# Kernel optimization log

Hardware: AMD Instinct MI355X
Metric: run time of the kernel (lower is better)

## Reference

```python
import jax, jax.numpy as jnp
import numpy as np

B, C, H, W = 64, 2048, 18, 9
INF = 1e9  # larger than any |cost| here (costs are -cosine sims in [-1,1])


def hungarian(cost):
    """Exact O(n^3) Jonker-Volgenant assignment (minimize total cost).
    cost: [n, n] float. Returns int32 [n]: column assigned to each row.
    Matches scipy.optimize.linear_sum_assignment on a square matrix.
    Uses 1-based indexing with a virtual row/column 0 (e-maxx formulation)."""
    n = cost.shape[0]
    costp = jnp.zeros((n + 1, n + 1), cost.dtype).at[1:, 1:].set(cost)
    jr = jnp.arange(n + 1)

    def assign_row(i, carry):
        u, v, p = carry          # u,v: dual potentials; p[j] = row matched to col j
        p = p.at[0].set(i)
        way0 = jnp.zeros(n + 1, jnp.int32)
        minv0 = jnp.full(n + 1, INF, cost.dtype)
        used0 = jnp.zeros(n + 1, bool)

        def cond(st):
            return ~st[6]

        def body(st):
            u, v, way, minv, used, j0, done = st
            used = used.at[j0].set(True)
            i0 = p[j0]
            cur = costp[i0] - u[i0] - v                  # reduced costs of row i0, vectorized over cols
            valid = (~used) & (jr >= 1)
            better = valid & (cur < minv)
            minv = jnp.where(better, cur, minv)
            way = jnp.where(better, j0, way)
            mv = jnp.where(valid, minv, INF)
            j1 = jnp.argmin(mv).astype(jnp.int32)
            delta = mv[j1]
            add = jnp.where(used, delta, jnp.zeros((), cost.dtype))
            u = u.at[p].add(add)                          # used cols have distinct p; unused add 0
            v = v - add
            minv = jnp.where(used, minv, minv - delta)
            return u, v, way, minv, used, j1, p[j1] == 0

        u, v, way, _, _, j0, _ = jax.lax.while_loop(
            cond, body, (u, v, way0, minv0, used0, jnp.int32(0), jnp.array(False)))

        def body2(st):
            j0, p = st
            j1 = way[j0]
            return j1, p.at[j0].set(p[j1])

        _, p = jax.lax.while_loop(lambda st: st[0] != 0, body2, (j0, p))
        return u, v, p

    u = jnp.zeros(n + 1, cost.dtype)
    v = jnp.zeros(n + 1, cost.dtype)
    p = jnp.zeros(n + 1, jnp.int32)
    u, v, p = jax.lax.fori_loop(1, n + 1, assign_row, (u, v, p))
    rowcol = jnp.zeros(n + 1, jnp.int32).at[p[1:]].set(jnp.arange(1, n + 1, dtype=jnp.int32))
    return rowcol[1:] - 1


def compute_mask(feat):
    b, c, h, w = feat.shape
    norms = jnp.linalg.norm(feat, axis=1).reshape(b, h * w)
    norms = norms - norms.min(axis=-1, keepdims=True)
    norms = norms / (norms.max(axis=-1, keepdims=True) + 1e-12)
    return jax.lax.stop_gradient(norms.reshape(b, 1, h, w))


def feature_similarity(fq, fk):
    b, c, h, w = fq.shape
    fq = fq.reshape(b, c, h * w)
    fk = fk.reshape(b, c, h * w)
    # F.normalize(dim=1): x / max(||x||, eps)
    nq = fq / jnp.maximum(jnp.linalg.norm(fq, axis=1, keepdims=True), 1e-12)
    nk = fk / jnp.maximum(jnp.linalg.norm(fk, axis=1, keepdims=True), 1e-12)
    return jnp.einsum('bcn,bcm->bnm', nq, nk)  # [b, n, n]


def setup_inputs() -> dict:
    key = jax.random.key(0)
    k1, k2, k3 = jax.random.split(key, 3)
    feat2d = jax.random.normal(k1, (B, C, H, W), dtype=jnp.float32)
    pos_ind = jax.random.randint(k2, (B,), 0, B, dtype=jnp.int64 if jax.config.jax_enable_x64 else jnp.int32).astype(jnp.int32)
    neg_ind = jax.random.randint(k3, (B,), 0, B, dtype=jnp.int32)
    return {"feat2d": feat2d, "pos_ind": pos_ind, "neg_ind": neg_ind}


def reference(feat2d, pos_ind, neg_ind):
    b, c, h, w = feat2d.shape
    n = h * w
    p = n // 2
    mask = compute_mask(feat2d)                         # [b,1,h,w], detached
    maskTr = mask.reshape(b, 1, n)
    s = jnp.sort(maskTr, axis=2)
    thr = s[:, :, p:p + 1]
    bMask = jnp.where(maskTr < thr, 0.0, 1.0).reshape(mask.shape)  # keep top half
    featMasked = feat2d * jax.lax.stop_gradient(bMask)
    featPos = feat2d[pos_ind]
    simPos = feature_similarity(featMasked, featPos)    # [b, n, n]
    # scipy linear_sum_assignment(sim, maximize=True) == minimize(-sim); indices are constants
    cols = jax.vmap(hungarian)(jax.lax.stop_gradient(-simPos))     # [b, n]
    assigned = jnp.take_along_axis(simPos, cols[:, :, None], axis=2)[..., 0]  # [b, n]
    pos_dis = 1.0 - assigned.sum(axis=-1) / p
    return jnp.mean(pos_dis)
```

## Files before the change

kernel.cpp:

```cpp
#include <hip/hip_runtime.h>
#include <hip/hip_bf16.h>

#define Bn 64
#define Cn 2048
#define Nn 162
#define Pn 81
#define NP 176
#define INFV 1.0e9f
#define BIGI 0x7FFFFFFF
#define RBW 328
#define ARRCAP 700

#define OFF_T    0
#define OFF_P    11534336
#define OFF_QS   (OFF_P + 64*32*192)
#define OFF_KS   (OFF_QS + 64*162)
#define OFF_COST (OFF_KS + 64*162)
#define OFF_PD   (OFF_COST + 64*162*162)

typedef __attribute__((ext_vector_type(8))) short bf16x8;
typedef __attribute__((ext_vector_type(4))) float f32x4;
typedef __attribute__((ext_vector_type(4))) unsigned u32x4;

static __device__ __forceinline__ unsigned short f2bf(float x) {
    unsigned int u = __builtin_bit_cast(unsigned int, x);
    unsigned int r = (u + 0x7fffu + ((u >> 16) & 1u)) >> 16;
    return (unsigned short)r;
}
static __device__ __forceinline__ unsigned short f2h(float x) {
    _Float16 h = (_Float16)x;
    return __builtin_bit_cast(unsigned short, h);
}
static __device__ __forceinline__ float h2f(unsigned short u) {
    return (float)__builtin_bit_cast(_Float16, u);
}
static __device__ __forceinline__ unsigned umin32(unsigned a, unsigned b) { return a < b ? a : b; }
static __device__ __forceinline__ unsigned umax32(unsigned a, unsigned b) { return a > b ? a : b; }
static __device__ __forceinline__ unsigned packnn(float v, int id) {
    float c = fmaxf(v, 0.f);
    return (__builtin_bit_cast(unsigned, c) & 0xFFFFFF00u) | (unsigned)id;
}
static __device__ __forceinline__ float unpacknn(unsigned pk) {
    return __builtin_bit_cast(float, pk & 0xFFFFFF00u);
}
static __device__ __forceinline__ unsigned reduceMin64(unsigned x) {
    int v = (int)x, t;
    t = __builtin_amdgcn_update_dpp(0, v, 0x121, 0xF, 0xF, true); v = (int)umin32((unsigned)v, (unsigned)t);
    t = __builtin_amdgcn_update_dpp(0, v, 0x122, 0xF, 0xF, true); v = (int)umin32((unsigned)v, (unsigned)t);
    t = __builtin_amdgcn_update_dpp(0, v, 0x124, 0xF, 0xF, true); v = (int)umin32((unsigned)v, (unsigned)t);
    t = __builtin_amdgcn_update_dpp(0, v, 0x128, 0xF, 0xF, true); v = (int)umin32((unsigned)v, (unsigned)t);
    unsigned a = (unsigned)__builtin_amdgcn_readlane(v, 0);
    unsigned b = (unsigned)__builtin_amdgcn_readlane(v, 16);
    unsigned c = (unsigned)__builtin_amdgcn_readlane(v, 32);
    unsigned d = (unsigned)__builtin_amdgcn_readlane(v, 48);
    return umin32(umin32(a, b), umin32(c, d));
}
static __device__ __forceinline__ int rlanei(int v, int l) { return __builtin_amdgcn_readlane(v, l); }
static __device__ __forceinline__ float rlanef(float v, int l) {
    return __builtin_bit_cast(float, __builtin_amdgcn_readlane(__builtin_bit_cast(int, v), l));
}
static __device__ __forceinline__ int laneOf(int id) { return id < 128 ? (id >> 1) : (id - 128); }
static __device__ __forceinline__ int slotOf(int id) { return id < 128 ? (id & 1) : 2; }
static __device__ __forceinline__ unsigned long long mask_n(int n) {
    if (n <= 0) return 0ull;
    if (n >= 64) return ~0ull;
    return (1ull << n) - 1ull;
}
#define SEL3(s, a0, a1, a2) ((s) == 0 ? (a0) : ((s) == 1 ? (a1) : (a2)))

__global__ __launch_bounds__(256) void k_tr(const float* __restrict__ feat, float* __restrict__ ws) {
    int x = blockIdx.x;
    int cc = x / 3, ct = x % 3;
    int b = blockIdx.y;
    int tid = threadIdx.x;
    int col = tid & 63, pg = tid >> 6;
    __shared__ unsigned Tp[32][65];
    __shared__ float Pp[4][64];
    int gc = ct * 64 + col;
    bool okc = (gc < Nn);
    const float* fbase = feat + ((size_t)b * Cn + (size_t)cc * 64) * Nn + gc;
    float s = 0.f;
    #pragma unroll
    for (int it = 0; it < 8; ++it) {
        int p = pg + it * 4;
        float v0 = okc ? fbase[(size_t)(2 * p) * Nn] : 0.f;
        float v1 = okc ? fbase[(size_t)(2 * p + 1) * Nn] : 0.f;
        s = fmaf(v0, v0, fmaf(v1, v1, s));
        Tp[p][col] = (unsigned)f2bf(v0) | ((unsigned)f2bf(v1) << 16);
    }
    Pp[pg][col] = s;
    __syncthreads();
    if (tid < 64) {
        float t0 = Pp[0][tid] + Pp[1][tid];
        float t1 = Pp[2][tid] + Pp[3][tid];
        ws[OFF_P + ((size_t)b * 32 + cc) * 192 + ct * 64 + tid] = t0 + t1;
    }
    unsigned* ft = (unsigned*)(ws + OFF_T);
    #pragma unroll
    for (int it = 0; it < 8; ++it) {
        int idx = it * 256 + tid;
        int c2 = idx >> 5, p = idx & 31;
        int gcol = ct * 64 + c2;
        if (gcol < NP) {
            ft[(size_t)(b * NP + gcol) * 1024 + cc * 32 + p] = Tp[p][c2];
        }
    }
}

__global__ void k_stats(float* __restrict__ ws) {
    int b = blockIdx.x;
    int t = threadIdx.x;
    __shared__ float arr[Nn];
    __shared__ float thr;
    float norm = 0.f;
    if (t < Nn) {
        float s = 0.f;
        #pragma unroll
        for (int ch = 0; ch < 32; ++ch) s += ws[OFF_P + ((size_t)b * 32 + ch) * 192 + t];
        norm = sqrtf(s);
        arr[t] = norm;
    }
    __syncthreads();
    float mn = INFV, mx = -INFV;
    for (int k = 0; k < Nn; ++k) { float v = arr[k]; mn = fminf(mn, v); mx = fmaxf(mx, v); }
    __syncthreads();
    float mval = 0.f;
    if (t < Nn) mval = (norm - mn) / (mx - mn + 1e-12f);
    __syncthreads();
    if (t < Nn) arr[t] = mval;
    __syncthreads();
    if (t < Nn) {
        int cl = 0, ce = 0, ceb = 0;
        for (int k = 0; k < Nn; ++k) {
            float v = arr[k];
            cl  += (v <  mval);
            ce  += (v == mval);
            ceb += (v == mval && k < t);
        }
        if (cl <= Pn && (cl + ce) > Pn && ceb == 0) thr = mval;
    }
    __syncthreads();
    if (t < Nn) {
        float inv = 1.f / fmaxf(norm, 1e-12f);
        ws[OFF_KS + (size_t)b * Nn + t] = inv;
        ws[OFF_QS + (size_t)b * Nn + t] = (mval < thr) ? 0.f : inv;
    }
}

__global__ __launch_bounds__(256) void k_mm(const int* __restrict__ pos_ind,
                                            float* __restrict__ ws) {
    int wg = blockIdx.x;
    int xcd = wg & 7, kk = wg >> 3;
    int b  = xcd + 8 * (kk / 11);
    int mt = kk % 11;
    int tid = threadIdx.x;
    int lane = tid & 63, w = tid >> 6;
    int q0 = mt * 16;
    int pb = pos_ind[b];
    const u32x4* At = (const u32x4*)((const unsigned short*)(ws + OFF_T) + (size_t)b  * NP * Cn);
    const u32x4* Bt = (const u32x4*)((const unsigned short*)(ws + OFF_T) + (size_t)pb * NP * Cn);
    __shared__ u32x4 As[16 * 16];
    __shared__ u32x4 Bs[192 * 16];

    f32x4 acc0 = {0.f, 0.f, 0.f, 0.f}, acc1 = acc0, acc2 = acc0;
    const int ct0 = w * 3, ct1 = w * 3 + 1, ct2 = w * 3 + 2;
    const int fr = lane & 15, fq = lane >> 4;

    for (int c0 = 0; c0 < Cn; c0 += 128) {
        int g0 = c0 >> 3;
        {
            int r = tid >> 4, g = tid & 15;
            As[r * 16 + (g ^ r)] = At[(size_t)(q0 + r) * 256 + g0 + g];
        }
        #pragma unroll
        for (int it = 0; it < 11; ++it) {
            int task = it * 256 + tid;
            int col = task >> 4, g = task & 15;
            Bs[col * 16 + (g ^ (col & 15))] = Bt[(size_t)col * 256 + g0 + g];
        }
        __syncthreads();
        #pragma unroll
        for (int ks = 0; ks < 4; ++ks) {
            int gk = ks * 4 + fq;
            bf16x8 af = *(const bf16x8*)&As[fr * 16 + (gk ^ fr)];
            bf16x8 b0 = *(const bf16x8*)&Bs[(ct0 * 16 + fr) * 16 + (gk ^ fr)];
            bf16x8 b1 = *(const bf16x8*)&Bs[(ct1 * 16 + fr) * 16 + (gk ^ fr)];
            bf16x8 b2 = *(const bf16x8*)&Bs[(ct2 * 16 + fr) * 16 + (gk ^ fr)];
            acc0 = __builtin_amdgcn_mfma_f32_16x16x32_bf16(af, b0, acc0, 0, 0, 0);
            acc1 = __builtin_amdgcn_mfma_f32_16x16x32_bf16(af, b1, acc1, 0, 0, 0);
            acc2 = __builtin_amdgcn_mfma_f32_16x16x32_bf16(af, b2, acc2, 0, 0, 0);
        }
        __syncthreads();
    }

    const float* qsv = ws + OFF_QS + (size_t)b  * Nn;
    const float* ksv = ws + OFF_KS + (size_t)pb * Nn;
    float* cost = ws + OFF_COST + (size_t)b * Nn * Nn;
    int c0_ = ct0 * 16 + fr, c1_ = ct1 * 16 + fr, c2_ = ct2 * 16 + fr;
    float ks0 = (c0_ < Nn) ? ksv[c0_] : 0.f;
    float ks1 = (c1_ < Nn) ? ksv[c1_] : 0.f;
    float ks2 = (c2_ < Nn) ? ksv[c2_] : 0.f;
    #pragma unroll
    for (int j = 0; j < 4; ++j) {
        int r = q0 + fq * 4 + j;
        if (r < Nn) {
            float qsr = qsv[r];
            if (c0_ < Nn) cost[(size_t)r * Nn + c0_] = -(acc0[j] * qsr * ks0);
            if (c1_ < Nn) cost[(size_t)r * Nn + c1_] = -(acc1[j] * qsr * ks1);
            if (c2_ < Nn) cost[(size_t)r * Nn + c2_] = -(acc2[j] * qsr * ks2);
        }
    }
}

__global__ __launch_bounds__(256) void k_hung(float* __restrict__ ws) {
    const int b = blockIdx.x;
    const int tid = threadIdx.x;
    const int lane = tid & 63, wv = tid >> 6;
    __shared__ unsigned short Cw[(Nn * RBW) / 2 + 32];
    __shared__ int rowBest[Nn + 1];
    __shared__ float Ulds[Nn + 1];
    __shared__ float dvA[192];
    __shared__ float pcm[4][192];
    __shared__ int   pim[4][192];
    __shared__ short rowIdxL[Nn];
    const float* cg  = ws + OFF_COST + (size_t)b * Nn * Nn;
    const float* qsv = ws + OFF_QS   + (size_t)b * Nn;

    const bool v2ok = (lane < Nn - 128);
    const int id0 = 2 * lane, id1 = 2 * lane + 1, id2 = 128 + lane;
    const int a32 = 4 * lane;
    const int a16 = 256 + 2 * lane;

    float q0 = qsv[lane];
    float q1 = qsv[64 + lane];
    float q2v = v2ok ? qsv[128 + lane] : 0.f;
    unsigned long long act0 = __ballot(q0 != 0.f);
    unsigned long long act1 = __ballot(q1 != 0.f);
    unsigned long long act2 = __ballot(v2ok && q2v != 0.f);
    int n0 = __popcll(act0), n1 = __popcll(act1), n2 = __popcll(act2);
    const int nact = n0 + n1 + n2;
    if (nact == 0) { if (tid == 0) ws[OFF_PD + b] = 1.f; return; }

    if (tid <= Nn) { rowBest[tid] = BIGI; Ulds[tid] = 0.f; }
    if (tid < 192) dvA[tid] = 0.f;
    if (wv == 0) {
        unsigned long long lt = (1ull << lane) - 1;
        if ((act0 >> lane) & 1) rowIdxL[__popcll(act0 & lt)] = (short)lane;
        if ((act1 >> lane) & 1) rowIdxL[n0 + __popcll(act1 & lt)] = (short)(64 + lane);
        if (v2ok && ((act2 >> lane) & 1)) rowIdxL[n0 + n1 + __popcll(act2 & lt)] = (short)(128 + lane);
    }
    __syncthreads();

    for (int k = wv; k < nact; k += 4) {
        int orig = rowIdxL[k];
        float2 f2 = *(const float2*)(cg + (size_t)orig * Nn + 2 * lane);
        unsigned pk = (unsigned)f2h(f2.x) | ((unsigned)f2h(f2.y) << 16);
        *(unsigned*)((char*)Cw + k * RBW + a32) = pk;
        if (v2ok) *(unsigned short*)((char*)Cw + k * RBW + a16) = f2h(cg[(size_t)orig * Nn + 128 + lane]);
    }
    __syncthreads();

    float cm0 = INFV, cm1 = INFV, cm2 = INFV; int im0 = 0, im1 = 0, im2 = 0;
    for (int k = wv; k < nact; k += 4) {
        unsigned pr = *(const unsigned*)((const char*)Cw + k * RBW + a32);
        float c0 = h2f((unsigned short)pr);
        float c1 = h2f((unsigned short)(pr >> 16));
        float c2 = h2f(*(const unsigned short*)((const char*)Cw + k * RBW + a16));
        if (c0 < cm0) { cm0 = c0; im0 = k + 1; }
        if (c1 < cm1) { cm1 = c1; im1 = k + 1; }
        if (v2ok && c2 < cm2) { cm2 = c2; im2 = k + 1; }
    }
    pcm[wv][id0] = cm0; pim[wv][id0] = im0;
    pcm[wv][id1] = cm1; pim[wv][id1] = im1;
    if (v2ok) { pcm[wv][id2] = cm2; pim[wv][id2] = im2; }
    __syncthreads();

    cm0 = INFV; im0 = 0; cm1 = INFV; im1 = 0; cm2 = INFV; im2 = 0;
    #pragma unroll
    for (int ww = 0; ww < 4; ++ww) {
        float c; int im;
        c = pcm[ww][id0]; im = pim[ww][id0];
        if (im > 0 && (im0 == 0 || c < cm0 || (c == cm0 && im < im0))) { cm0 = c; im0 = im; }
        c = pcm[ww][id1]; im = pim[ww][id1];
        if (im > 0 && (im1 == 0 || c < cm1 || (c == cm1 && im < im1))) { cm1 = c; im1 = im; }
        if (v2ok) {
            c = pcm[ww][id2]; im = pim[ww][id2];
            if (im > 0 && (im2 == 0 || c < cm2 || (c == cm2 && im < im2))) { cm2 = c; im2 = im; }
        }
    }
    if (wv == 0) {
        if (im0 > 0) atomicMin(&rowBest[im0], id0);
        if (im1 > 0) atomicMin(&rowBest[im1], id1);
        if (v2ok && im2 > 0) atomicMin(&rowBest[im2], id2);
    }
    __syncthreads();

    float v0 = cm0, v1 = cm1, v2 = v2ok ? cm2 : 0.f;
    int Pa0 = (im0 > 0 && rowBest[im0] == id0) ? im0 : 0;
    int Pa1 = (im1 > 0 && rowBest[im1] == id1) ? im1 : 0;
    int Pa2 = (v2ok && im2 > 0 && rowBest[im2] == id2) ? im2 : 0;

    unsigned long long cb0 = __ballot(lane + 1 <= nact && rowBest[lane + 1] != BIGI);
    unsigned long long cb1 = __ballot(lane + 65 <= nact && rowBest[lane + 65] != BIGI);
    unsigned long long cb2 = __ballot(lane + 129 <= nact && rowBest[lane + 129] != BIGI);
    unsigned long long fr0 = mask_n(nact)       & ~cb0;
    unsigned long long fr1 = mask_n(nact - 64)  & ~cb1;
    unsigned long long fr2 = mask_n(nact - 128) & ~cb2;

    for (int k = wv; k < nact; k += 4) {
        int j1c = rowBest[k + 1];
        if (j1c == BIGI) continue;
        int roff = k * RBW;
        unsigned pr = *(const unsigned*)((const char*)Cw + roff + a32);
        float r0 = h2f((unsigned short)pr) - v0;
        float r1 = h2f((unsigned short)(pr >> 16)) - v1;
        float r2 = h2f(*(const unsigned short*)((const char*)Cw + roff + a16)) - v2;
        unsigned p0 = (id0 == j1c) ? 0xFFFFFFFFu : packnn(r0, id0);
        unsigned p1 = (id1 == j1c) ? 0xFFFFFFFFu : packnn(r1, id1);
        unsigned p2 = (v2ok && id2 != j1c) ? packnn(r2, id2) : 0xFFFFFFFFu;
        unsigned pk = reduceMin64(umin32(p0, umin32(p1, p2)));
        float min2 = unpacknn(pk);
        if (lane == 0) { dvA[j1c] = min2; Ulds[k + 1] = min2; }
    }
    __syncthreads();
    if (wv != 0) return;

    float ur0, ur1, ur2;
    v0 -= dvA[id0]; ur0 = dvA[id0];
    v1 -= dvA[id1]; ur1 = dvA[id1];
    if (v2ok) { v2 -= dvA[id2]; ur2 = dvA[id2]; } else ur2 = 0.f;

    float minv0 = INFV, minv1 = INFV, minv2 = INFV;
    int way0 = 255, way1 = 255, way2 = 255;
    bool used0 = false, used1 = false, used2 = false;

    unsigned long long nx0 = 0, nx1 = 0, nx2 = 0;
    int arrIt = 0;
    for (int pass = 0; pass < 2; ++pass) {
        while ((fr0 | fr1 | fr2) != 0 && arrIt < ARRCAP) {
            ++arrIt;
            int i;
            if (fr0)      { int t = __builtin_ctzll(fr0); i = t + 1;   fr0 &= fr0 - 1; }
            else if (fr1) { int t = __builtin_ctzll(fr1); i = t + 65;  fr1 &= fr1 - 1; }
            else          { int t = __builtin_ctzll(fr2); i = t + 129; fr2 &= fr2 - 1; }
            int roff = (i - 1) * RBW;
            unsigned pr = *(const unsigned*)((const char*)Cw + roff + a32);
            float r0 = h2f((unsigned short)pr) - v0;
            float r1 = h2f((unsigned short)(pr >> 16)) - v1;
            float r2 = h2f(*(const unsigned short*)((const char*)Cw + roff + a16)) - v2;
            unsigned p0 = packnn(r0, id0);
            unsigned p1 = packnn(r1, id1);
            unsigned p2 = v2ok ? packnn(r2, id2) : 0xFFFFFFFFu;
            unsigned lmin = umin32(p0, umin32(p1, p2));
            unsigned lmed = umin32(umax32(p0, p1), umax32(umin32(p0, p1), p2));
            unsigned M1 = reduceMin64(lmin);
            unsigned M2 = reduceMin64(lmin == M1 ? lmed : lmin);
            int j1 = (int)(M1 & 0xFFu), j2 = (int)(M2 & 0xFFu);
            int l1 = laneOf(j1), s1 = slotOf(j1);
            int l2 = laneOf(j2), s2 = slotOf(j2);
            float umin_e = rlanef(SEL3(s1, r0, r1, r2), l1);
            float usub_e = rlanef(SEL3(s2, r0, r1, r2), l2);
            int iA = rlanei(SEL3(s1, Pa0, Pa1, Pa2), l1);
            int iB = rlanei(SEL3(s2, Pa0, Pa1, Pa2), l2);
            if (usub_e < umin_e) {
                int tj = j1; j1 = j2; j2 = tj;
                int tl = l1; l1 = l2; l2 = tl;
                int ts = s1; s1 = s2; s2 = ts;
                float tv = umin_e; umin_e = usub_e; usub_e = tv;
                int ti = iA; iA = iB; iB = ti;
            }
            bool strict = (umin_e < usub_e);
            int jt, idisp;
            float ua = usub_e;
            if (strict) {
                float d = usub_e - umin_e;
                if (lane == l1) { if (s1 == 0) v0 -= d; else if (s1 == 1) v1 -= d; else v2 -= d; }
                jt = j1; idisp = iA;
            } else if (iA > 0) {
                jt = j2; idisp = iB;
            } else {
                jt = j1; idisp = 0;
            }
            int lt = laneOf(jt), st = slotOf(jt);
            if (lane == lt) {
                if (st == 0)      { Pa0 = i; ur0 = ua; }
                else if (st == 1) { Pa1 = i; ur1 = ua; }
                else              { Pa2 = i; ur2 = ua; }
            }
            if (lane == 0) Ulds[i] = ua;
            if (idisp > 0) {
                if (strict) {
                    if (idisp <= 64)       fr0 |= 1ull << (idisp - 1);
                    else if (idisp <= 128) fr1 |= 1ull << (idisp - 65);
                    else                   fr2 |= 1ull << (idisp - 129);
                } else {
                    if (idisp <= 64)       nx0 |= 1ull << (idisp - 1);
                    else if (idisp <= 128) nx1 |= 1ull << (idisp - 65);
                    else                   nx2 |= 1ull << (idisp - 129);
                }
            }
        }
        fr0 |= nx0; fr1 |= nx1; fr2 |= nx2;
        nx0 = nx1 = nx2 = 0;
    }

    while ((fr0 | fr1 | fr2) != 0) {
        int i;
        if (fr0)      { int t = __builtin_ctzll(fr0); i = t + 1;   fr0 &= fr0 - 1; }
        else if (fr1) { int t = __builtin_ctzll(fr1); i = t + 65;  fr1 &= fr1 - 1; }
        else          { int t = __builtin_ctzll(fr2); i = t + 129; fr2 &= fr2 - 1; }
        float u_root = Ulds[i];
        minv0 = minv1 = minv2 = INFV;
        way0 = way1 = way2 = 255;
        used0 = used1 = used2 = false;
        {
            int roff = (i - 1) * RBW;
            unsigned pr = *(const unsigned*)((const char*)Cw + roff + a32);
            float c0 = h2f((unsigned short)pr);
            float c1 = h2f((unsigned short)(pr >> 16));
            float c2 = h2f(*(const unsigned short*)((const char*)Cw + roff + a16));
            minv0 = c0 - (u_root + v0);
            minv1 = c1 - (u_root + v1);
            minv2 = v2ok ? (c2 - (u_root + v2)) : INFV;
        }
        int jend = -1;
        for (int it = 0; it < Nn + 2; ++it) {
            unsigned q0p = used0 ? 0xFFFFFFFFu : packnn(minv0, id0);
            unsigned q1p = used1 ? 0xFFFFFFFFu : packnn(minv1, id1);
            unsigned q2p = (v2ok && !used2) ? packnn(minv2, id2) : 0xFFFFFFFFu;
            unsigned pk = reduceMin64(umin32(q0p, umin32(q1p, q2p)));
            int j1 = (int)(pk & 0xFFu);
            float delta = unpacknn(pk);
            int l1 = laneOf(j1), s1 = slotOf(j1);
            int i1 = rlanei(SEL3(s1, Pa0, Pa1, Pa2), l1);
            float u1 = rlanef(SEL3(s1, ur0, ur1, ur2), l1);
            u_root += delta;
            v0 = used0 ? v0 - delta : v0;  ur0 = used0 ? ur0 + delta : ur0;  minv0 = used0 ? minv0 : minv0 - delta;
            v1 = used1 ? v1 - delta : v1;  ur1 = used1 ? ur1 + delta : ur1;  minv1 = used1 ? minv1 : minv1 - delta;
            v2 = used2 ? v2 - delta : v2;  ur2 = used2 ? ur2 + delta : ur2;  minv2 = used2 ? minv2 : minv2 - delta;
            bool hit = (lane == l1);
            if (s1 == 0) used0 |= hit; else if (s1 == 1) used1 |= hit; else used2 |= hit;
            if (i1 == 0) { jend = j1; break; }
            int roff = (i1 - 1) * RBW;
            unsigned pr = *(const unsigned*)((const char*)Cw + roff + a32);
            float c0 = h2f((unsigned short)pr);
            float c1 = h2f((unsigned short)(pr >> 16));
            float c2 = h2f(*(const unsigned short*)((const char*)Cw + roff + a16));
            float n0 = c0 - (u1 + v0), n1 = c1 - (u1 + v1), n2 = c2 - (u1 + v2);
            if (!used0 && n0 < minv0) { minv0 = n0; way0 = j1; }
            if (!used1 && n1 < minv1) { minv1 = n1; way1 = j1; }
            if (v2ok && !used2 && n2 < minv2) { minv2 = n2; way2 = j1; }
        }
        int j = jend;
        while (j >= 0) {
            int l = laneOf(j), s = slotOf(j);
            int w = rlanei(SEL3(s, way0, way1, way2), l);
            int pnew; float unew;
            if (w == 255) { pnew = i; unew = u_root; }
            else {
                int lw = laneOf(w), sw = slotOf(w);
                pnew = rlanei(SEL3(sw, Pa0, Pa1, Pa2), lw);
                unew = rlanef(SEL3(sw, ur0, ur1, ur2), lw);
            }
            if (lane == l) {
                if (s == 0)      { Pa0 = pnew; ur0 = unew; }
                else if (s == 1) { Pa1 = pnew; ur1 = unew; }
                else             { Pa2 = pnew; ur2 = unew; }
            }
            j = (w == 255) ? -1 : w;
        }
    }

    float tot = 0.f;
    if (Pa0 > 0) { int orig = rowIdxL[Pa0 - 1]; tot -= cg[(size_t)orig * Nn + id0]; }
    if (Pa1 > 0) { int orig = rowIdxL[Pa1 - 1]; tot -= cg[(size_t)orig * Nn + id1]; }
    if (v2ok && Pa2 > 0) { int orig = rowIdxL[Pa2 - 1]; tot -= cg[(size_t)orig * Nn + id2]; }
    #pragma unroll
    for (int off = 32; off; off >>= 1) tot += __shfl_xor(tot, off);
    if (lane == 0) ws[OFF_PD + b] = 1.f - tot * (1.f / (float)Pn);
}

__global__ void k_final(const float* __restrict__ ws, float* __restrict__ out) {
    float v = ws[OFF_PD + threadIdx.x];
    #pragma unroll
    for (int off = 32; off; off >>= 1) v += __shfl_xor(v, off);
    if (threadIdx.x == 0) out[0] = v * (1.f / 64.f);
}

extern "C" void kernel_launch(void* const* d_in, const int* in_sizes, int n_in,
                              void* d_out, int out_size, void* d_ws, size_t ws_size,
                              hipStream_t stream) {
    const float* feat = (const float*)d_in[0];
    const int*   pos  = (const int*)d_in[1];
    float* ws  = (float*)d_ws;
    float* out = (float*)d_out;
    k_tr   <<<dim3(96, 64), 256, 0, stream>>>(feat, ws);
    k_stats<<<64, 192, 0, stream>>>(ws);
    k_mm   <<<704, 256, 0, stream>>>(pos, ws);
    k_hung <<<64, 256, 0, stream>>>(ws);
    k_final<<<1, 64, 0, stream>>>(ws, out);
}
```

Measured before the change: 108.7 us.

## Fuse norm/threshold stats into Hungarian kernel, enlarge matmul row tile, vectorize transpose loads

```diff
diff --git a/kernel.cpp b/kernel.cpp
--- a/kernel.cpp
+++ b/kernel.cpp
@@ -73,77 +73,46 @@
     int cc = x / 3, ct = x % 3;
     int b = blockIdx.y;
     int tid = threadIdx.x;
-    int col = tid & 63, pg = tid >> 6;
+    int c2 = tid & 31, pg = tid >> 5;
     __shared__ unsigned Tp[32][65];
-    __shared__ float Pp[4][64];
-    int gc = ct * 64 + col;
-    bool okc = (gc < Nn);
-    const float* fbase = feat + ((size_t)b * Cn + (size_t)cc * 64) * Nn + gc;
-    float s = 0.f;
+    __shared__ float Pp[8][64];
+    int gc0 = ct * 64 + 2 * c2;
+    bool ok  = (gc0 < Nn);
+    bool ok1 = (gc0 + 1 < Nn);
+    const float* fb = feat + ((size_t)b * Cn + (size_t)cc * 64) * Nn;
+    float s0 = 0.f, s1 = 0.f;
     #pragma unroll
-    for (int it = 0; it < 8; ++it) {
-        int p = pg + it * 4;
-        float v0 = okc ? fbase[(size_t)(2 * p) * Nn] : 0.f;
-        float v1 = okc ? fbase[(size_t)(2 * p + 1) * Nn] : 0.f;
-        s = fmaf(v0, v0, fmaf(v1, v1, s));
-        Tp[p][col] = (unsigned)f2bf(v0) | ((unsigned)f2bf(v1) << 16);
-    }
-    Pp[pg][col] = s;
+    for (int it = 0; it < 4; ++it) {
+        int p = pg + it * 8;
+        float2 fa = {0.f, 0.f}, fc = {0.f, 0.f};
+        if (ok) {
+            fa = *(const float2*)(fb + (size_t)(2 * p) * Nn + gc0);
+            fc = *(const float2*)(fb + (size_t)(2 * p + 1) * Nn + gc0);
+            if (!ok1) { fa.y = 0.f; fc.y = 0.f; }
+        }
+        s0 = fmaf(fa.x, fa.x, fmaf(fc.x, fc.x, s0));
+        s1 = fmaf(fa.y, fa.y, fmaf(fc.y, fc.y, s1));
+        Tp[p][2 * c2]     = (unsigned)f2bf(fa.x) | ((unsigned)f2bf(fc.x) << 16);
+        Tp[p][2 * c2 + 1] = (unsigned)f2bf(fa.y) | ((unsigned)f2bf(fc.y) << 16);
+    }
+    Pp[pg][2 * c2]     = s0;
+    Pp[pg][2 * c2 + 1] = s1;
     __syncthreads();
     if (tid < 64) {
-        float t0 = Pp[0][tid] + Pp[1][tid];
-        float t1 = Pp[2][tid] + Pp[3][tid];
-        ws[OFF_P + ((size_t)b * 32 + cc) * 192 + ct * 64 + tid] = t0 + t1;
+        float t = 0.f;
+        #pragma unroll
+        for (int g = 0; g < 8; ++g) t += Pp[g][tid];
+        ws[OFF_P + ((size_t)b * 32 + cc) * 192 + ct * 64 + tid] = t;
     }
     unsigned* ft = (unsigned*)(ws + OFF_T);
     #pragma unroll
     for (int it = 0; it < 8; ++it) {
         int idx = it * 256 + tid;
-        int c2 = idx >> 5, p = idx & 31;
-        int gcol = ct * 64 + c2;
+        int c = idx >> 5, p = idx & 31;
+        int gcol = ct * 64 + c;
         if (gcol < NP) {
-            ft[(size_t)(b * NP + gcol) * 1024 + cc * 32 + p] = Tp[p][c2];
-        }
-    }
-}
-
-__global__ void k_stats(float* __restrict__ ws) {
-    int b = blockIdx.x;
-    int t = threadIdx.x;
-    __shared__ float arr[Nn];
-    __shared__ float thr;
-    float norm = 0.f;
-    if (t < Nn) {
-        float s = 0.f;
-        #pragma unroll
-        for (int ch = 0; ch < 32; ++ch) s += ws[OFF_P + ((size_t)b * 32 + ch) * 192 + t];
-        norm = sqrtf(s);
-        arr[t] = norm;
-    }
-    __syncthreads();
-    float mn = INFV, mx = -INFV;
-    for (int k = 0; k < Nn; ++k) { float v = arr[k]; mn = fminf(mn, v); mx = fmaxf(mx, v); }
-    __syncthreads();
-    float mval = 0.f;
-    if (t < Nn) mval = (norm - mn) / (mx - mn + 1e-12f);
-    __syncthreads();
-    if (t < Nn) arr[t] = mval;
-    __syncthreads();
-    if (t < Nn) {
-        int cl = 0, ce = 0, ceb = 0;
-        for (int k = 0; k < Nn; ++k) {
-            float v = arr[k];
-            cl  += (v <  mval);
-            ce  += (v == mval);
-            ceb += (v == mval && k < t);
-        }
-        if (cl <= Pn && (cl + ce) > Pn && ceb == 0) thr = mval;
-    }
-    __syncthreads();
-    if (t < Nn) {
-        float inv = 1.f / fmaxf(norm, 1e-12f);
-        ws[OFF_KS + (size_t)b * Nn + t] = inv;
-        ws[OFF_QS + (size_t)b * Nn + t] = (mval < thr) ? 0.f : inv;
+            ft[(size_t)(b * NP + gcol) * 1024 + cc * 32 + p] = Tp[p][c];
+        }
     }
 }
 
@@ -151,63 +120,71 @@
                                             float* __restrict__ ws) {
     int wg = blockIdx.x;
     int xcd = wg & 7, kk = wg >> 3;
-    int b  = xcd + 8 * (kk / 11);
-    int mt = kk % 11;
+    int b  = xcd + 8 * (kk / 6);
+    int mt = kk % 6;
     int tid = threadIdx.x;
     int lane = tid & 63, w = tid >> 6;
-    int q0 = mt * 16;
+    int q0 = mt * 32;
     int pb = pos_ind[b];
     const u32x4* At = (const u32x4*)((const unsigned short*)(ws + OFF_T) + (size_t)b  * NP * Cn);
     const u32x4* Bt = (const u32x4*)((const unsigned short*)(ws + OFF_T) + (size_t)pb * NP * Cn);
-    __shared__ u32x4 As[16 * 16];
+    __shared__ u32x4 As[32 * 16];
     __shared__ u32x4 Bs[192 * 16];
 
-    f32x4 acc0 = {0.f, 0.f, 0.f, 0.f}, acc1 = acc0, acc2 = acc0;
+    f32x4 a00 = {0.f, 0.f, 0.f, 0.f}, a01 = a00, a02 = a00, a10 = a00, a11 = a00, a12 = a00;
     const int ct0 = w * 3, ct1 = w * 3 + 1, ct2 = w * 3 + 2;
     const int fr = lane & 15, fq = lane >> 4;
 
     for (int c0 = 0; c0 < Cn; c0 += 128) {
         int g0 = c0 >> 3;
-        {
-            int r = tid >> 4, g = tid & 15;
-            As[r * 16 + (g ^ r)] = At[(size_t)(q0 + r) * 256 + g0 + g];
-        }
         #pragma unroll
-        for (int it = 0; it < 11; ++it) {
+        for (int it = 0; it < 2; ++it) {
+            int task = it * 256 + tid;
+            int r = task >> 4, g = task & 15;
+            int rowc = q0 + r; if (rowc > NP - 1) rowc = NP - 1;
+            As[r * 16 + (g ^ (r & 15))] = At[(size_t)rowc * 256 + g0 + g];
+        }
+        #pragma unroll
+        for (int it = 0; it < 12; ++it) {
             int task = it * 256 + tid;
             int col = task >> 4, g = task & 15;
-            Bs[col * 16 + (g ^ (col & 15))] = Bt[(size_t)col * 256 + g0 + g];
+            int rowc = col; if (rowc > NP - 1) rowc = NP - 1;
+            Bs[col * 16 + (g ^ (col & 15))] = Bt[(size_t)rowc * 256 + g0 + g];
         }
         __syncthreads();
         #pragma unroll
         for (int ks = 0; ks < 4; ++ks) {
             int gk = ks * 4 + fq;
-            bf16x8 af = *(const bf16x8*)&As[fr * 16 + (gk ^ fr)];
+            bf16x8 af0 = *(const bf16x8*)&As[fr * 16 + (gk ^ fr)];
+            bf16x8 af1 = *(const bf16x8*)&As[(16 + fr) * 16 + (gk ^ fr)];
             bf16x8 b0 = *(const bf16x8*)&Bs[(ct0 * 16 + fr) * 16 + (gk ^ fr)];
             bf16x8 b1 = *(const bf16x8*)&Bs[(ct1 * 16 + fr) * 16 + (gk ^ fr)];
             bf16x8 b2 = *(const bf16x8*)&Bs[(ct2 * 16 + fr) * 16 + (gk ^ fr)];
-            acc0 = __builtin_amdgcn_mfma_f32_16x16x32_bf16(af, b0, acc0, 0, 0, 0);
-            acc1 = __builtin_amdgcn_mfma_f32_16x16x32_bf16(af, b1, acc1, 0, 0, 0);
-            acc2 = __builtin_amdgcn_mfma_f32_16x16x32_bf16(af, b2, acc2, 0, 0, 0);
+            a00 = __builtin_amdgcn_mfma_f32_16x16x32_bf16(af0, b0, a00, 0, 0, 0);
+            a01 = __builtin_amdgcn_mfma_f32_16x16x32_bf16(af0, b1, a01, 0, 0, 0);
+            a02 = __builtin_amdgcn_mfma_f32_16x16x32_bf16(af0, b2, a02, 0, 0, 0);
+            a10 = __builtin_amdgcn_mfma_f32_16x16x32_bf16(af1, b0, a10, 0, 0, 0);
+            a11 = __builtin_amdgcn_mfma_f32_16x16x32_bf16(af1, b1, a11, 0, 0, 0);
+            a12 = __builtin_amdgcn_mfma_f32_16x16x32_bf16(af1, b2, a12, 0, 0, 0);
         }
         __syncthreads();
     }
 
-    const float* qsv = ws + OFF_QS + (size_t)b  * Nn;
-    const float* ksv = ws + OFF_KS + (size_t)pb * Nn;
-    float* cost = ws + OFF_COST + (size_t)b * Nn * Nn;
+    float* simg = ws + OFF_COST + (size_t)b * Nn * Nn;
     int c0_ = ct0 * 16 + fr, c1_ = ct1 * 16 + fr, c2_ = ct2 * 16 + fr;
-    float ks0 = (c0_ < Nn) ? ksv[c0_] : 0.f;
-    float ks1 = (c1_ < Nn) ? ksv[c1_] : 0.f;
-    float ks2 = (c2_ < Nn) ? ksv[c2_] : 0.f;
     #pragma unroll
     for (int j = 0; j < 4; ++j) {
-        int r = q0 + fq * 4 + j;
-        if (r < Nn) {
-            float qsr = qsv[r];
-            if (c0_ < Nn) cost[(size_t)r * Nn + c0_] = -(acc0[j] * qsr * ks0);
-            if (c1_ < Nn) cost[(size_t)r * Nn + c1_] = -(acc1[j] * qsr * ks1);
-            if (c2_ < Nn) cost[(size_t)r * Nn + c2_] = -(acc2[j] * qsr * ks2);
+        int r0 = q0 + fq * 4 + j;
+        int r1 = r0 + 16;
+        if (r0 < Nn) {
+            if (c0_ < Nn) simg[(size_t)r0 * Nn + c0_] = a00[j];
+            if (c1_ < Nn) simg[(size_t)r0 * Nn + c1_] = a01[j];
+            if (c2_ < Nn) simg[(size_t)r0 * Nn + c2_] = a02[j];
+        }
+        if (r1 < Nn) {
+            if (c0_ < Nn) simg[(size_t)r1 * Nn + c0_] = a10[j];
+            if (c1_ < Nn) simg[(size_t)r1 * Nn + c1_] = a11[j];
+            if (c2_ < Nn) simg[(size_t)r1 * Nn + c2_] = a12[j];
         }
     }
 }
@@ -223,26 +200,70 @@
     __shared__ float pcm[4][192];
     __shared__ int   pim[4][192];
     __shared__ short rowIdxL[Nn];
-    const float* cg  = ws + OFF_COST + (size_t)b * Nn * Nn;
-    const float* qsv = ws + OFF_QS   + (size_t)b * Nn;
+    __shared__ float qsL[192];
+    __shared__ float ksL[192];
+    const float* cg = ws + OFF_COST + (size_t)b * Nn * Nn;
 
     const bool v2ok = (lane < Nn - 128);
     const int id0 = 2 * lane, id1 = 2 * lane + 1, id2 = 128 + lane;
     const int a32 = 4 * lane;
     const int a16 = 256 + 2 * lane;
 
-    float q0 = qsv[lane];
-    float q1 = qsv[64 + lane];
-    float q2v = v2ok ? qsv[128 + lane] : 0.f;
-    unsigned long long act0 = __ballot(q0 != 0.f);
-    unsigned long long act1 = __ballot(q1 != 0.f);
-    unsigned long long act2 = __ballot(v2ok && q2v != 0.f);
+    if (tid <= Nn) { rowBest[tid] = BIGI; Ulds[tid] = 0.f; }
+    if (tid < 192) dvA[tid] = 0.f;
+
+    float* arrS = &pcm[0][0];
+    float* thrP = &pcm[1][0];
+    float normv = 0.f, mvalv = 0.f;
+    if (tid < Nn) {
+        float s = 0.f;
+        #pragma unroll
+        for (int ch = 0; ch < 32; ++ch) s += ws[OFF_P + ((size_t)b * 32 + ch) * 192 + tid];
+        normv = sqrtf(s);
+        arrS[tid] = normv;
+    }
+    __syncthreads();
+    {
+        float mn = INFV, mx = -INFV;
+        for (int k = 0; k < Nn; ++k) { float v = arrS[k]; mn = fminf(mn, v); mx = fmaxf(mx, v); }
+        if (tid < Nn) mvalv = (normv - mn) / (mx - mn + 1e-12f);
+    }
+    __syncthreads();
+    if (tid < Nn) arrS[tid] = mvalv;
+    __syncthreads();
+    if (tid < Nn) {
+        int cl = 0, ce = 0, ceb = 0;
+        for (int k = 0; k < Nn; ++k) {
+            float v = arrS[k];
+            cl  += (v <  mvalv);
+            ce  += (v == mvalv);
+            ceb += (v == mvalv && k < tid);
+        }
+        if (cl <= Pn && (cl + ce) > Pn && ceb == 0) thrP[0] = mvalv;
+    }
+    if (tid < 192) { qsL[tid] = 0.f; ksL[tid] = 0.f; }
+    __syncthreads();
+    if (tid < Nn) {
+        float inv = 1.f / fmaxf(normv, 1e-12f);
+        ksL[tid] = inv;
+        qsL[tid] = (mvalv < thrP[0]) ? 0.f : inv;
+    }
+    __syncthreads();
+
+    const float ks0f = ksL[id0];
+    const float ks1f = ksL[id1];
+    const float ks2f = v2ok ? ksL[id2] : 0.f;
+
+    float aq0 = qsL[lane];
+    float aq1 = qsL[64 + lane];
+    float aq2 = v2ok ? qsL[128 + lane] : 0.f;
+    unsigned long long act0 = __ballot(aq0 != 0.f);
+    unsigned long long act1 = __ballot(aq1 != 0.f);
+    unsigned long long act2 = __ballot(v2ok && aq2 != 0.f);
     int n0 = __popcll(act0), n1 = __popcll(act1), n2 = __popcll(act2);
     const int nact = n0 + n1 + n2;
     if (nact == 0) { if (tid == 0) ws[OFF_PD + b] = 1.f; return; }
 
-    if (tid <= Nn) { rowBest[tid] = BIGI; Ulds[tid] = 0.f; }
-    if (tid < 192) dvA[tid] = 0.f;
     if (wv == 0) {
         unsigned long long lt = (1ull << lane) - 1;
         if ((act0 >> lane) & 1) rowIdxL[__popcll(act0 & lt)] = (short)lane;
@@ -253,10 +274,13 @@
 
     for (int k = wv; k < nact; k += 4) {
         int orig = rowIdxL[k];
+        float qsr = qsL[orig];
         float2 f2 = *(const float2*)(cg + (size_t)orig * Nn + 2 * lane);
-        unsigned pk = (unsigned)f2h(f2.x) | ((unsigned)f2h(f2.y) << 16);
+        unsigned pk = (unsigned)f2h(-(f2.x * qsr * ks0f))
+                    | ((unsigned)f2h(-(f2.y * qsr * ks1f)) << 16);
         *(unsigned*)((char*)Cw + k * RBW + a32) = pk;
-        if (v2ok) *(unsigned short*)((char*)Cw + k * RBW + a16) = f2h(cg[(size_t)orig * Nn + 128 + lane]);
+        if (v2ok) *(unsigned short*)((char*)Cw + k * RBW + a16) =
+            f2h(-(cg[(size_t)orig * Nn + 128 + lane] * qsr * ks2f));
     }
     __syncthreads();
 
@@ -446,10 +470,10 @@
             float c0 = h2f((unsigned short)pr);
             float c1 = h2f((unsigned short)(pr >> 16));
             float c2 = h2f(*(const unsigned short*)((const char*)Cw + roff + a16));
-            float n0 = c0 - (u1 + v0), n1 = c1 - (u1 + v1), n2 = c2 - (u1 + v2);
-            if (!used0 && n0 < minv0) { minv0 = n0; way0 = j1; }
-            if (!used1 && n1 < minv1) { minv1 = n1; way1 = j1; }
-            if (v2ok && !used2 && n2 < minv2) { minv2 = n2; way2 = j1; }
+            float n0_ = c0 - (u1 + v0), n1_ = c1 - (u1 + v1), n2_ = c2 - (u1 + v2);
+            if (!used0 && n0_ < minv0) { minv0 = n0_; way0 = j1; }
+            if (!used1 && n1_ < minv1) { minv1 = n1_; way1 = j1; }
+            if (v2ok && !used2 && n2_ < minv2) { minv2 = n2_; way2 = j1; }
         }
         int j = jend;
         while (j >= 0) {
@@ -472,9 +496,9 @@
     }
 
     float tot = 0.f;
-    if (Pa0 > 0) { int orig = rowIdxL[Pa0 - 1]; tot -= cg[(size_t)orig * Nn + id0]; }
-    if (Pa1 > 0) { int orig = rowIdxL[Pa1 - 1]; tot -= cg[(size_t)orig * Nn + id1]; }
-    if (v2ok && Pa2 > 0) { int orig = rowIdxL[Pa2 - 1]; tot -= cg[(size_t)orig * Nn + id2]; }
+    if (Pa0 > 0) { int orig = rowIdxL[Pa0 - 1]; tot += cg[(size_t)orig * Nn + id0] * qsL[orig] * ks0f; }
+    if (Pa1 > 0) { int orig = rowIdxL[Pa1 - 1]; tot += cg[(size_t)orig * Nn + id1] * qsL[orig] * ks1f; }
+    if (v2ok && Pa2 > 0) { int orig = rowIdxL[Pa2 - 1]; tot += cg[(size_t)orig * Nn + id2] * qsL[orig] * ks2f; }
     #pragma unroll
     for (int off = 32; off; off >>= 1) tot += __shfl_xor(tot, off);
     if (lane == 0) ws[OFF_PD + b] = 1.f - tot * (1.f / (float)Pn);
@@ -495,8 +519,7 @@
     float* ws  = (float*)d_ws;
     float* out = (float*)d_out;
     k_tr   <<<dim3(96, 64), 256, 0, stream>>>(feat, ws);
-    k_stats<<<64, 192, 0, stream>>>(ws);
-    k_mm   <<<704, 256, 0, stream>>>(pos, ws);
+    k_mm   <<<384, 256, 0, stream>>>(pos, ws);
     k_hung <<<64, 256, 0, stream>>>(ws);
     k_final<<<1, 64, 0, stream>>>(ws, out);
 }
```

New measurement: 103.6 us. -4.7%, faster.
